# Performance work log

Measured on AMD Instinct MI355X. Metric: run time of the kernel, lower is better.

The kernel has to match this reference:

```python
import jax, jax.numpy as jnp
import numpy as np

MIDC = 256
HEADS = 16
HEADC = MIDC // HEADS
EPS = 1e-5


def _layernorm(x, w, b):
    # Faithful to the custom torch LayerNorm: unbiased std (ddof=1) and
    # division by (std + eps), NOT sqrt(var + eps).
    mean = jnp.mean(x, axis=-1, keepdims=True)
    std = jnp.std(x, axis=-1, keepdims=True, ddof=1)
    return w * (x - mean) / (std + EPS) + b


def setup_inputs() -> dict:
    key = jax.random.key(0)
    ks = jax.random.split(key, 3)
    B, HW = 8, 16384
    x = jax.random.normal(ks[0], (B, HW, MIDC), dtype=jnp.float32)
    W_qkv = jax.random.normal(ks[1], (3 * MIDC, MIDC), dtype=jnp.float32) * 0.02
    b_qkv = jnp.zeros((3 * MIDC,), dtype=jnp.float32)
    kln_w = jnp.ones((HEADS, 1, HEADC), dtype=jnp.float32)
    kln_b = jnp.zeros((HEADS, 1, HEADC), dtype=jnp.float32)
    vln_w = jnp.ones((HEADS, 1, HEADC), dtype=jnp.float32)
    vln_b = jnp.zeros((HEADS, 1, HEADC), dtype=jnp.float32)
    W_proj = jax.random.normal(ks[2], (MIDC, MIDC), dtype=jnp.float32) * 0.02
    b_proj = jnp.zeros((MIDC,), dtype=jnp.float32)
    return {"x": x, "W_qkv": W_qkv, "b_qkv": b_qkv,
            "kln_w": kln_w, "kln_b": kln_b, "vln_w": vln_w, "vln_b": vln_b,
            "W_proj": W_proj, "b_proj": b_proj}


def reference(x, W_qkv, b_qkv, kln_w, kln_b, vln_w, vln_b, W_proj, b_proj):
    B, HW, C = x.shape
    bias = x
    # QKV projection -> [B, heads, HW, 3*headc]
    qkv = (jnp.einsum('bnc,oc->bno', x, W_qkv) + b_qkv)
    qkv = qkv.reshape(B, HW, HEADS, 3 * HEADC).transpose(0, 2, 1, 3)
    q, k, v = jnp.split(qkv, 3, axis=-1)  # each [B, heads, HW, headc]
    k = _layernorm(k, kln_w, kln_b)
    v = _layernorm(v, vln_w, vln_b)
    # linear attention: kv = k^T v / HW, then q @ kv
    kv = jnp.einsum('bhnd,bhne->bhde', k, v) / HW  # [B, heads, headc, headc]
    out = jnp.einsum('bhnd,bhde->bhne', q, kv)     # [B, heads, HW, headc]
    out = out.transpose(0, 2, 1, 3).reshape(B, HW, C)
    ret = out + bias
    proj = jnp.einsum('bnc,oc->bno', ret, W_proj) + b_proj
    return jax.nn.gelu(proj, approximate=False) + bias
```

## Files before the change

kernel.cpp:

```cpp
#include <hip/hip_runtime.h>
#include <hip/hip_bf16.h>
#include <math.h>


#define EPSF 1e-5f

typedef __bf16 bf16x8 __attribute__((ext_vector_type(8)));
typedef __bf16 bf16x4 __attribute__((ext_vector_type(4)));
typedef float  f32x4  __attribute__((ext_vector_type(4)));

__global__ void k0_prep(const float* __restrict__ Wqkv, const float* __restrict__ Wproj,
                        __bf16* __restrict__ Wkv, __bf16* __restrict__ Wp,
                        float* __restrict__ kv) {
  int idx = blockIdx.x * 256 + threadIdx.x;
  if (idx < 32768) kv[idx] = 0.f;
  {
    int r = idx >> 8, c = idx & 255;
    int half = r >> 8;
    int rr = r & 255;
    int h = rr >> 4, d = rr & 15;
    Wkv[idx] = (__bf16)Wqkv[(h*48 + 16 + half*16 + d)*256 + c];
  }
  if (idx < 65536) Wp[idx] = (__bf16)Wproj[idx];
}

__launch_bounds__(512, 4)
__global__ void k1a(const float* __restrict__ x, const __bf16* __restrict__ Wkv,
                    const float* __restrict__ bqkv,
                    const float* __restrict__ klnw, const float* __restrict__ klnb,
                    const float* __restrict__ vlnw, const float* __restrict__ vlnb,
                    float* __restrict__ kvout) {
  __shared__ __align__(16) char smem[70656];
  __bf16 (*xs)[264] = reinterpret_cast<__bf16(*)[264]>(smem);
  const int tid = threadIdx.x;
  const int w = tid >> 6, l = tid & 63, lr = l & 15, g = l >> 4;
  __bf16 (*tTk)[72] = reinterpret_cast<__bf16(*)[72]>(smem + 33792 + w*4608);
  __bf16 (*tTv)[64] = reinterpret_cast<__bf16(*)[64]>(smem + w*4096);

  const long row0 = (long)blockIdx.x * 64;
  const int b = (int)(row0 >> 14);

  #pragma unroll
  for (int i = 0; i < 8; ++i) {
    int idx = tid + i*512;
    int r = idx >> 6, c4 = (idx & 63) << 2;
    f32x4 v = *reinterpret_cast<const f32x4*>(x + (row0 + r)*256 + c4);
    bf16x4 pk; pk[0]=(__bf16)v[0]; pk[1]=(__bf16)v[1]; pk[2]=(__bf16)v[2]; pk[3]=(__bf16)v[3];
    *reinterpret_cast<bf16x4*>(&xs[r][c4]) = pk;
  }

  bf16x8 wk[2][8];
  #pragma unroll
  for (int cb=0;cb<2;cb++) {
    const __bf16* wp = Wkv + (size_t)(w*32 + cb*16 + lr)*256 + g*8;
    #pragma unroll
    for (int kc=0;kc<8;kc++) wk[cb][kc] = *reinterpret_cast<const bf16x8*>(wp + kc*32);
  }
  __syncthreads();

  f32x4 acc[2][4];
  for (int cb=0;cb<2;cb++) for (int rb=0;rb<4;rb++)
    for (int j=0;j<4;j++) acc[cb][rb][j]=0.f;
  #pragma unroll
  for (int kc = 0; kc < 8; ++kc) {
    const int kb = kc*32 + g*8;
    bf16x8 bf_[4];
    #pragma unroll
    for (int rb=0;rb<4;rb++)
      bf_[rb] = *reinterpret_cast<const bf16x8*>(&xs[rb*16+lr][kb]);
    #pragma unroll
    for (int cb=0;cb<2;cb++)
      #pragma unroll
      for (int rb=0;rb<4;rb++)
        acc[cb][rb] = __builtin_amdgcn_mfma_f32_16x16x32_bf16(wk[cb][kc], bf_[rb], acc[cb][rb], 0,0,0);
  }

  bf16x8 wv[2][8];
  #pragma unroll
  for (int cb=0;cb<2;cb++) {
    const __bf16* wp = Wkv + (size_t)(256 + w*32 + cb*16 + lr)*256 + g*8;
    #pragma unroll
    for (int kc=0;kc<8;kc++) wv[cb][kc] = *reinterpret_cast<const bf16x8*>(wp + kc*32);
  }

  #pragma unroll
  for (int cb=0;cb<2;cb++) {
    const int h = 2*w + cb;
    const f32x4 bb  = *reinterpret_cast<const f32x4*>(bqkv + h*48 + 16 + 4*g);
    const f32x4 lwv = *reinterpret_cast<const f32x4*>(klnw + h*16 + 4*g);
    const f32x4 lbv = *reinterpret_cast<const f32x4*>(klnb + h*16 + 4*g);
    #pragma unroll
    for (int rb=0;rb<4;rb++) {
      float v0 = acc[cb][rb][0] + bb[0];
      float v1 = acc[cb][rb][1] + bb[1];
      float v2 = acc[cb][rb][2] + bb[2];
      float v3 = acc[cb][rb][3] + bb[3];
      float sum = v0+v1+v2+v3;
      sum += __shfl_xor(sum, 16); sum += __shfl_xor(sum, 32);
      const float mu = sum * 0.0625f;
      const float d0=v0-mu, d1=v1-mu, d2=v2-mu, d3=v3-mu;
      float q = d0*d0 + d1*d1 + d2*d2 + d3*d3;
      q += __shfl_xor(q, 16); q += __shfl_xor(q, 32);
      const float sc = 1.f/(sqrtf(q*(1.f/15.f)) + EPSF);
      const int rr = rb*16 + lr;
      tTk[cb*16 + 4*g+0][rr] = (__bf16)(lwv[0]*d0*sc + lbv[0]);
      tTk[cb*16 + 4*g+1][rr] = (__bf16)(lwv[1]*d1*sc + lbv[1]);
      tTk[cb*16 + 4*g+2][rr] = (__bf16)(lwv[2]*d2*sc + lbv[2]);
      tTk[cb*16 + 4*g+3][rr] = (__bf16)(lwv[3]*d3*sc + lbv[3]);
    }
  }

  for (int cb=0;cb<2;cb++) for (int rb=0;rb<4;rb++)
    for (int j=0;j<4;j++) acc[cb][rb][j]=0.f;
  #pragma unroll
  for (int kc = 0; kc < 8; ++kc) {
    const int kb = kc*32 + g*8;
    bf16x8 bf_[4];
    #pragma unroll
    for (int rb=0;rb<4;rb++)
      bf_[rb] = *reinterpret_cast<const bf16x8*>(&xs[rb*16+lr][kb]);
    #pragma unroll
    for (int cb=0;cb<2;cb++)
      #pragma unroll
      for (int rb=0;rb<4;rb++)
        acc[cb][rb] = __builtin_amdgcn_mfma_f32_16x16x32_bf16(wv[cb][kc], bf_[rb], acc[cb][rb], 0,0,0);
  }
  __syncthreads();

  #pragma unroll
  for (int cb=0;cb<2;cb++) {
    const int h = 2*w + cb;
    const f32x4 bb  = *reinterpret_cast<const f32x4*>(bqkv + h*48 + 32 + 4*g);
    const f32x4 lwv = *reinterpret_cast<const f32x4*>(vlnw + h*16 + 4*g);
    const f32x4 lbv = *reinterpret_cast<const f32x4*>(vlnb + h*16 + 4*g);
    #pragma unroll
    for (int rb=0;rb<4;rb++) {
      float v0 = acc[cb][rb][0] + bb[0];
      float v1 = acc[cb][rb][1] + bb[1];
      float v2 = acc[cb][rb][2] + bb[2];
      float v3 = acc[cb][rb][3] + bb[3];
      float sum = v0+v1+v2+v3;
      sum += __shfl_xor(sum, 16); sum += __shfl_xor(sum, 32);
      const float mu = sum * 0.0625f;
      const float d0=v0-mu, d1=v1-mu, d2=v2-mu, d3=v3-mu;
      float q = d0*d0 + d1*d1 + d2*d2 + d3*d3;
      q += __shfl_xor(q, 16); q += __shfl_xor(q, 32);
      const float sc = 1.f/(sqrtf(q*(1.f/15.f)) + EPSF);
      const int rr = rb*16 + lr;
      tTv[cb*16 + 4*g+0][rr ^ (((4*g+0)&7)<<3)] = (__bf16)(lwv[0]*d0*sc + lbv[0]);
      tTv[cb*16 + 4*g+1][rr ^ (((4*g+1)&7)<<3)] = (__bf16)(lwv[1]*d1*sc + lbv[1]);
      tTv[cb*16 + 4*g+2][rr ^ (((4*g+2)&7)<<3)] = (__bf16)(lwv[2]*d2*sc + lbv[2]);
      tTv[cb*16 + 4*g+3][rr ^ (((4*g+3)&7)<<3)] = (__bf16)(lwv[3]*d3*sc + lbv[3]);
    }
  }

  #pragma unroll
  for (int hh=0; hh<2; ++hh) {
    f32x4 c; c[0]=0.f; c[1]=0.f; c[2]=0.f; c[3]=0.f;
    #pragma unroll
    for (int ch=0; ch<2; ++ch) {
      const int s = ch*32 + g*8;
      bf16x8 a  = *reinterpret_cast<const bf16x8*>(&tTk[hh*16 + lr][s]);
      bf16x8 bv = *reinterpret_cast<const bf16x8*>(&tTv[hh*16 + lr][s ^ ((lr&7)<<3)]);
      c = __builtin_amdgcn_mfma_f32_16x16x32_bf16(a, bv, c, 0,0,0);
    }
    float* dst = kvout + ((size_t)(b*16 + 2*w + hh) << 8);
    #pragma unroll
    for (int j=0;j<4;j++)
      atomicAdd(dst + (4*g+j)*16 + lr, c[j]);
  }
}

__global__ void k2_weff(const float* __restrict__ Wqkv, const float* __restrict__ bqkv,
                        const float* __restrict__ kvin,
                        __bf16* __restrict__ Wqe, float* __restrict__ beff) {
  const int b = blockIdx.x >> 4, h = blockIdx.x & 15;
  const int c = threadIdx.x;
  __shared__ float kvs[16][16];
  kvs[c >> 4][c & 15] = kvin[(b*16 + h)*256 + c] * (1.f/16384.f);
  __syncthreads();
  #pragma unroll 4
  for (int e=0;e<16;e++) {
    float acc = 0.f;
    #pragma unroll
    for (int d=0; d<16; d++)
      acc += kvs[d][e] * Wqkv[(h*48 + d)*256 + c];
    Wqe[((size_t)b*256 + h*16 + e)*256 + c] = (__bf16)acc;
  }
  if (c < 16) {
    float acc = 0.f;
    #pragma unroll
    for (int d=0; d<16; d++) acc += kvs[d][c] * bqkv[h*48 + d];
    beff[b*256 + h*16 + c] = acc;
  }
}

__launch_bounds__(512, 4)
__global__ void k3_fused(const float* __restrict__ x, const __bf16* __restrict__ Wqe,
                         const float* __restrict__ beff, const __bf16* __restrict__ Wp,
                         const float* __restrict__ bproj, float* __restrict__ out) {
  __shared__ __align__(16) __bf16 xs[64][264];
  __shared__ __align__(16) __bf16 rs[64][264];
  const int tid = threadIdx.x;
  const long browg = (long)blockIdx.x * 64;
  const int b = (int)(browg >> 14);
  const int w = tid>>6, l = tid&63, lr = l&15, g = l>>4;

  #pragma unroll
  for (int i = 0; i < 8; ++i) {
    int idx = tid + i*512;
    int r = idx >> 6, c4 = (idx & 63) << 2;
    f32x4 v = *reinterpret_cast<const f32x4*>(x + (browg + r)*256 + c4);
    bf16x4 pk; pk[0]=(__bf16)v[0]; pk[1]=(__bf16)v[1]; pk[2]=(__bf16)v[2]; pk[3]=(__bf16)v[3];
    *reinterpret_cast<bf16x4*>(&xs[r][c4]) = pk;
  }

  const __bf16* Bq = Wqe + (size_t)b*65536;
  bf16x8 wq[2][8];
  #pragma unroll
  for (int cb=0;cb<2;cb++) {
    const __bf16* wp = Bq + (size_t)(w*32 + cb*16 + lr)*256 + g*8;
    #pragma unroll
    for (int kc=0;kc<8;kc++) wq[cb][kc] = *reinterpret_cast<const bf16x8*>(wp + kc*32);
  }
  __syncthreads();

  f32x4 acc[2][4];
  for (int cb=0;cb<2;cb++) for (int rb=0;rb<4;rb++)
    for (int j=0;j<4;j++) acc[cb][rb][j]=0.f;
  #pragma unroll
  for (int kc=0;kc<8;kc++) {
    const int kb = kc*32 + g*8;
    bf16x8 bf_[4];
    #pragma unroll
    for (int rb=0;rb<4;rb++)
      bf_[rb] = *reinterpret_cast<const bf16x8*>(&xs[rb*16+lr][kb]);
    #pragma unroll
    for (int cb=0;cb<2;cb++)
      #pragma unroll
      for (int rb=0;rb<4;rb++)
        acc[cb][rb] = __builtin_amdgcn_mfma_f32_16x16x32_bf16(wq[cb][kc], bf_[rb], acc[cb][rb], 0,0,0);
  }

  bf16x8 wpj[2][8];
  #pragma unroll
  for (int cb=0;cb<2;cb++) {
    const __bf16* wp = Wp + (size_t)(w*32 + cb*16 + lr)*256 + g*8;
    #pragma unroll
    for (int kc=0;kc<8;kc++) wpj[cb][kc] = *reinterpret_cast<const bf16x8*>(wp + kc*32);
  }

  #pragma unroll
  for (int cb=0;cb<2;cb++) {
    const int c0 = w*32 + cb*16 + 4*g;
    const f32x4 be = *reinterpret_cast<const f32x4*>(beff + b*256 + c0);
    #pragma unroll
    for (int rb=0;rb<4;rb++) {
      const int r = rb*16 + lr;
      bf16x4 xv = *reinterpret_cast<const bf16x4*>(&xs[r][c0]);
      bf16x4 pk;
      #pragma unroll
      for (int j=0;j<4;j++)
        pk[j] = (__bf16)(acc[cb][rb][j] + be[j] + (float)xv[j]);
      *reinterpret_cast<bf16x4*>(&rs[r][c0]) = pk;
    }
  }
  __syncthreads();

  f32x4 acc2[2][4];
  for (int cb=0;cb<2;cb++) for (int rb=0;rb<4;rb++)
    for (int j=0;j<4;j++) acc2[cb][rb][j]=0.f;
  #pragma unroll
  for (int kc=0;kc<8;kc++) {
    const int kb = kc*32 + g*8;
    bf16x8 bf_[4];
    #pragma unroll
    for (int rb=0;rb<4;rb++)
      bf_[rb] = *reinterpret_cast<const bf16x8*>(&rs[rb*16+lr][kb]);
    #pragma unroll
    for (int cb=0;cb<2;cb++)
      #pragma unroll
      for (int rb=0;rb<4;rb++)
        acc2[cb][rb] = __builtin_amdgcn_mfma_f32_16x16x32_bf16(wpj[cb][kc], bf_[rb], acc2[cb][rb], 0,0,0);
  }

  #pragma unroll
  for (int cb=0;cb<2;cb++) {
    const int c0 = w*32 + cb*16 + 4*g;
    const f32x4 bp4 = *reinterpret_cast<const f32x4*>(bproj + c0);
    #pragma unroll
    for (int rb=0;rb<4;rb++) {
      const long gr = browg + rb*16 + lr;
      const f32x4 xv = *reinterpret_cast<const f32x4*>(x + gr*256 + c0);
      f32x4 o;
      #pragma unroll
      for (int j=0;j<4;j++) {
        float z = acc2[cb][rb][j] + bp4[j];
        o[j] = 0.5f*z*(1.f + erff(z*0.70710678118f)) + xv[j];
      }
      *reinterpret_cast<f32x4*>(out + gr*256 + c0) = o;
    }
  }
}

extern "C" void kernel_launch(void* const* d_in, const int* in_sizes, int n_in,
                              void* d_out, int out_size, void* d_ws, size_t ws_size,
                              hipStream_t stream) {
  const float* x    = (const float*)d_in[0];
  const float* Wqkv = (const float*)d_in[1];
  const float* bqkv = (const float*)d_in[2];
  const float* klnw = (const float*)d_in[3];
  const float* klnb = (const float*)d_in[4];
  const float* vlnw = (const float*)d_in[5];
  const float* vlnb = (const float*)d_in[6];
  const float* Wproj= (const float*)d_in[7];
  const float* bproj= (const float*)d_in[8];
  float* out = (float*)d_out;

  char* ws = (char*)d_ws;
  __bf16* Wkv = (__bf16*)(ws);
  __bf16* Wp  = (__bf16*)(ws + 262144);
  float*  kv  = (float*) (ws + 393216);
  __bf16* Wqe = (__bf16*)(ws + 524288);
  float*  beff= (float*) (ws + 1572864);

  k0_prep <<<512, 256, 0, stream>>>(Wqkv, Wproj, Wkv, Wp, kv);
  k1a     <<<2048, 512, 0, stream>>>(x, Wkv, bqkv, klnw, klnb, vlnw, vlnb, kv);
  k2_weff <<<128, 256, 0, stream>>>(Wqkv, bqkv, kv, Wqe, beff);
  k3_fused<<<2048, 512, 0, stream>>>(x, Wqe, beff, Wp, bproj, out);
}
```

Before: 212.8 us.

## Stage GELU output through shared memory for coalesced stores; use rsqrt in layernorm

```diff
diff --git a/kernel.cpp b/kernel.cpp
--- a/kernel.cpp
+++ b/kernel.cpp
@@ -101,7 +101,7 @@
       const float d0=v0-mu, d1=v1-mu, d2=v2-mu, d3=v3-mu;
       float q = d0*d0 + d1*d1 + d2*d2 + d3*d3;
       q += __shfl_xor(q, 16); q += __shfl_xor(q, 32);
-      const float sc = 1.f/(sqrtf(q*(1.f/15.f)) + EPSF);
+      const float sc = __frsqrt_rn(q * (1.f/15.f));
       const int rr = rb*16 + lr;
       tTk[cb*16 + 4*g+0][rr] = (__bf16)(lwv[0]*d0*sc + lbv[0]);
       tTk[cb*16 + 4*g+1][rr] = (__bf16)(lwv[1]*d1*sc + lbv[1]);
@@ -145,7 +145,7 @@
       const float d0=v0-mu, d1=v1-mu, d2=v2-mu, d3=v3-mu;
       float q = d0*d0 + d1*d1 + d2*d2 + d3*d3;
       q += __shfl_xor(q, 16); q += __shfl_xor(q, 32);
-      const float sc = 1.f/(sqrtf(q*(1.f/15.f)) + EPSF);
+      const float sc = __frsqrt_rn(q * (1.f/15.f));
       const int rr = rb*16 + lr;
       tTv[cb*16 + 4*g+0][rr ^ (((4*g+0)&7)<<3)] = (__bf16)(lwv[0]*d0*sc + lbv[0]);
       tTv[cb*16 + 4*g+1][rr ^ (((4*g+1)&7)<<3)] = (__bf16)(lwv[1]*d1*sc + lbv[1]);
@@ -200,7 +200,9 @@
                          const float* __restrict__ beff, const __bf16* __restrict__ Wp,
                          const float* __restrict__ bproj, float* __restrict__ out) {
   __shared__ __align__(16) __bf16 xs[64][264];
-  __shared__ __align__(16) __bf16 rs[64][264];
+  __shared__ __align__(16) char rsraw[33792];
+  __bf16 (*rs)[264] = reinterpret_cast<__bf16(*)[264]>(rsraw);
+  float  (*fst)[260] = reinterpret_cast<float(*)[260]>(rsraw);
   const int tid = threadIdx.x;
   const long browg = (long)blockIdx.x * 64;
   const int b = (int)(browg >> 14);
@@ -283,23 +285,37 @@
       for (int rb=0;rb<4;rb++)
         acc2[cb][rb] = __builtin_amdgcn_mfma_f32_16x16x32_bf16(wpj[cb][kc], bf_[rb], acc2[cb][rb], 0,0,0);
   }
-
-  #pragma unroll
-  for (int cb=0;cb<2;cb++) {
-    const int c0 = w*32 + cb*16 + 4*g;
-    const f32x4 bp4 = *reinterpret_cast<const f32x4*>(bproj + c0);
-    #pragma unroll
-    for (int rb=0;rb<4;rb++) {
-      const long gr = browg + rb*16 + lr;
-      const f32x4 xv = *reinterpret_cast<const f32x4*>(x + gr*256 + c0);
-      f32x4 o;
-      #pragma unroll
-      for (int j=0;j<4;j++) {
-        float z = acc2[cb][rb][j] + bp4[j];
-        o[j] = 0.5f*z*(1.f + erff(z*0.70710678118f)) + xv[j];
+  __syncthreads();
+
+  #pragma unroll
+  for (int half=0; half<2; ++half) {
+    #pragma unroll
+    for (int cb=0;cb<2;cb++) {
+      const int c0 = w*32 + cb*16 + 4*g;
+      const f32x4 bp4 = *reinterpret_cast<const f32x4*>(bproj + c0);
+      #pragma unroll
+      for (int rbh=0;rbh<2;rbh++) {
+        const int rb = half*2 + rbh;
+        const int r = rb*16 + lr;
+        bf16x4 xv = *reinterpret_cast<const bf16x4*>(&xs[r][c0]);
+        f32x4 o;
+        #pragma unroll
+        for (int j=0;j<4;j++) {
+          float z = acc2[cb][rb][j] + bp4[j];
+          o[j] = 0.5f*z*(1.f + erff(z*0.70710678118f)) + (float)xv[j];
+        }
+        *reinterpret_cast<f32x4*>(&fst[r - half*32][c0]) = o;
       }
-      *reinterpret_cast<f32x4*>(out + gr*256 + c0) = o;
-    }
+    }
+    __syncthreads();
+    #pragma unroll
+    for (int i=0;i<4;i++) {
+      int idx = tid + i*512;
+      int r32 = idx >> 6, c4 = (idx & 63) << 2;
+      f32x4 v = *reinterpret_cast<const f32x4*>(&fst[r32][c4]);
+      *reinterpret_cast<f32x4*>(out + (browg + half*32 + r32)*256 + c4) = v;
+    }
+    if (half == 0) __syncthreads();
   }
 }
 
```

New measurement: 193.2 us. 9.2% less time.
